# Kernel optimization log

Hardware: AMD Instinct MI355X
Metric: run time of the kernel (lower is better)

## Reference

```python
import jax, jax.numpy as jnp
import numpy as np

# Multi-level grid resolutions (module constants from init_kwargs)
RESO_3D = [16, 32, 64]
RESO_2D = [64, 128, 256]
EPS = 1e-9


def _corners(D):
    # binary corner offsets, shape (2**D, D)
    c = np.stack(np.meshgrid(*([np.arange(2)] * D), indexing='ij'), axis=-1).reshape(-1, D)
    return jnp.asarray(c, dtype=jnp.int32)


def _coords_weights(xyz, reso):
    # xyz in [0,1), shape (N, D). Returns flat voxel idx (N, 2**D) and trilinear weights (N, 2**D).
    D = xyz.shape[1]
    corners = _corners(D)                                   # (C, D)
    x = xyz * (reso - 1)
    x0 = jnp.floor(x)
    frac = x - x0                                           # (N, D)
    x0 = x0.astype(jnp.int32)
    cc = jnp.clip(x0[:, None, :] + corners[None], 0, reso - 1)   # (N, C, D)
    w = jnp.prod(jnp.where(corners[None] == 1, frac[:, None, :], 1.0 - frac[:, None, :]), axis=-1)  # (N, C)
    strides = (reso ** jnp.arange(D - 1, -1, -1)).astype(jnp.int32)  # row-major
    idx = jnp.sum(cc * strides, axis=-1)                    # (N, C)
    return idx, w


def _grid_create(xyz, feat, reso):
    # Scatter-splat: weighted-average point features into a dense level grid (reso**D, F).
    N, D = xyz.shape
    F = feat.shape[1]
    idx, w = _coords_weights(xyz, reso)                     # (N, C)
    flat_idx = idx.reshape(-1)
    wf = jnp.zeros((reso ** D, F), dtype=feat.dtype).at[flat_idx].add(
        (w[..., None] * feat[:, None, :]).reshape(-1, F))
    ws = jnp.zeros((reso ** D,), dtype=feat.dtype).at[flat_idx].add(w.reshape(-1))
    return wf / jnp.maximum(ws, EPS)[:, None]


def _grid_encode(xyz, grid, reso):
    # Gather + trilinear interpolation from a dense level grid. Returns (M, F).
    idx, w = _coords_weights(xyz, reso)                     # (M, C)
    vals = grid[idx]                                        # (M, C, F)
    return jnp.sum(w[..., None] * vals, axis=1)


def _spatial_ctx(xyz_c, xyz_i, feat):
    outs = []
    # 3D multi-level grid
    for R in RESO_3D:
        g = _grid_create(xyz_c, feat, R)
        outs.append(_grid_encode(xyz_i, g, R))
    # triplane 2D grids: xy, xz, yz
    for dims in ((0, 1), (0, 2), (1, 2)):
        xc = xyz_c[:, list(dims)]
        xi = xyz_i[:, list(dims)]
        for R in RESO_2D:
            g = _grid_create(xc, feat, R)
            outs.append(_grid_encode(xi, g, R))
    return jnp.concatenate(outs, axis=-1)  # (M, (L3 + 3*L2) * F)


def setup_inputs() -> dict:
    key = jax.random.key(0)
    k1, k2, k3 = jax.random.split(key, 3)
    N, M, F = 200000, 100000, 32
    xyz_for_creater = jax.random.uniform(k1, (N, 3), dtype=jnp.float32)
    xyz_for_interp = jax.random.uniform(k2, (M, 3), dtype=jnp.float32)
    feature = jax.random.normal(k3, (N, F), dtype=jnp.float32)
    return {"xyz_for_creater": xyz_for_creater,
            "xyz_for_interp": xyz_for_interp,
            "feature": feature}


def reference(xyz_for_creater, xyz_for_interp, feature):
    return _spatial_ctx(xyz_for_creater, xyz_for_interp, feature)
```

## Files before the change

kernel.cpp:

```cpp
#include <hip/hip_runtime.h>

#define NF 32
#define EPSF 1e-9f

#define KSORT 458752
#define VO16 0
#define VO32 4096
#define VO64Q 36864
#define VO128Q 49152
#define KVIS2 98304
#define KO16 0
#define KO32 4096
#define KO64 36864
#define KO64Q 299008
#define KO128Q 311296
#define KO256Q 360448
#define KVIS 557056

__device__ __forceinline__ int cell_coord(float xv, int R, float& fr) {
  float x = xv * (float)(R - 1);
  int i0 = (int)floorf(x);
  i0 = min(max(i0, 0), R - 2);
  fr = x - (float)i0;
  return i0;
}
__device__ __forceinline__ float bf2f(unsigned short u) {
  return __uint_as_float((unsigned)u << 16);
}
__device__ __forceinline__ unsigned short f2bf(float x) {
  unsigned b = __float_as_uint(x);
  return (unsigned short)((b + 0x7FFF + ((b >> 16) & 1)) >> 16);
}
__device__ __forceinline__ unsigned p1b2(unsigned x) {
  x &= 0x3FF;
  x = (x | (x << 16)) & 0x030000FF;
  x = (x | (x << 8)) & 0x0300F00F;
  x = (x | (x << 4)) & 0x030C30C3;
  x = (x | (x << 2)) & 0x09249249;
  return x;
}
__device__ __forceinline__ unsigned p1b1(unsigned x) {
  x &= 0xFFFF;
  x = (x | (x << 8)) & 0x00FF00FF;
  x = (x | (x << 4)) & 0x0F0F0F0F;
  x = (x | (x << 2)) & 0x33333333;
  x = (x | (x << 1)) & 0x55555555;
  return x;
}
__device__ __forceinline__ unsigned c1b2(unsigned x) {
  x &= 0x09249249u;
  x = (x | (x >> 2)) & 0x030C30C3u;
  x = (x | (x >> 4)) & 0x0300F00Fu;
  x = (x | (x >> 8)) & 0x030000FFu;
  x = (x | (x >> 16)) & 0x3FFu;
  return x;
}
__device__ __forceinline__ unsigned c1b1(unsigned x) {
  x &= 0x55555555u;
  x = (x | (x >> 1)) & 0x33333333u;
  x = (x | (x >> 2)) & 0x0F0F0F0Fu;
  x = (x | (x >> 4)) & 0x00FF00FFu;
  x = (x | (x >> 8)) & 0xFFFFu;
  return x;
}

__device__ __forceinline__ int xcd_swz(int bid, int n) {
  return (bid & 7) * (n >> 3) + (bid >> 3);
}

__device__ __forceinline__ void agg_hist(int key, int* cnt) {
  int lane = threadIdx.x & 63;
  unsigned long long amask = __ballot(1);
  int nact = __popcll(amask);
  int prev = __shfl_up(key, 1);
  bool leader = (lane == 0) || (prev != key);
  unsigned long long lmask = __ballot(leader);
  if (leader) {
    unsigned long long above = (lane < 63) ? (lmask >> (lane + 1)) : 0ULL;
    int next = above ? (lane + 1 + (__ffsll((unsigned long long)above) - 1)) : nact;
    atomicAdd(&cnt[key], next - lane);
  }
}
template <int NC>
__device__ __forceinline__ void agg_place_batch(const int (&key)[NC], int* cur,
                                                int (&pos)[NC]) {
  int lane = threadIdx.x & 63;
  unsigned long long amask = __ballot(1);
  int nact = __popcll(amask);
  int ret[NC];
  int lp[NC];
#pragma unroll
  for (int c = 0; c < NC; ++c) {
    int prev = __shfl_up(key[c], 1);
    bool leader = (lane == 0) || (prev != key[c]);
    unsigned long long lmask = __ballot(leader);
    unsigned long long below = lmask & ((2ULL << lane) - 1ULL);
    lp[c] = 63 - __clzll((long long)below);
    ret[c] = 0;
    if (leader) {
      unsigned long long above = (lane < 63) ? (lmask >> (lane + 1)) : 0ULL;
      int next = above ? (lane + 1 + (__ffsll((unsigned long long)above) - 1)) : nact;
      ret[c] = atomicAdd(&cur[key[c]], next - lane);
    }
  }
#pragma unroll
  for (int c = 0; c < NC; ++c) pos[c] = __shfl(ret[c], lp[c]) + (lane - lp[c]);
}

__global__ __launch_bounds__(256) void sort_hist_all(
    const float* __restrict__ xyz, int* __restrict__ cnt, int N) {
  int p = blockIdx.x * blockDim.x + threadIdx.x;
  if (p >= N) return;
  float fr;
  int c64[3], c256[3];
#pragma unroll
  for (int d = 0; d < 3; ++d) {
    c64[d] = cell_coord(xyz[p * 3 + d], 64, fr);
    c256[d] = cell_coord(xyz[p * 3 + d], 256, fr);
  }
  int k3 = (int)((p1b2((unsigned)c64[0]) << 2) | (p1b2((unsigned)c64[1]) << 1) |
                 p1b2((unsigned)c64[2]));
  atomicAdd(&cnt[k3], 1);
#pragma unroll
  for (int g = 0; g < 3; ++g) {
    int a = (g < 2) ? 0 : 1, b = (g == 0) ? 1 : 2;
    int key = 262144 + g * 65536 +
              (int)((p1b1((unsigned)c256[a]) << 1) | p1b1((unsigned)c256[b]));
    atomicAdd(&cnt[key], 1);
  }
}
__global__ __launch_bounds__(256) void sort_place_all(
    const float* __restrict__ xyz, int* __restrict__ cur, int* __restrict__ perm, int N) {
  int p = blockIdx.x * blockDim.x + threadIdx.x;
  if (p >= N) return;
  float fr;
  int c64[3], c256[3];
#pragma unroll
  for (int d = 0; d < 3; ++d) {
    c64[d] = cell_coord(xyz[p * 3 + d], 64, fr);
    c256[d] = cell_coord(xyz[p * 3 + d], 256, fr);
  }
  int k3 = (int)((p1b2((unsigned)c64[0]) << 2) | (p1b2((unsigned)c64[1]) << 1) |
                 p1b2((unsigned)c64[2]));
  perm[atomicAdd(&cur[k3], 1)] = p;
#pragma unroll
  for (int g = 0; g < 3; ++g) {
    int a = (g < 2) ? 0 : 1, b = (g == 0) ? 1 : 2;
    int key = 262144 + g * 65536 +
              (int)((p1b1((unsigned)c256[a]) << 1) | p1b1((unsigned)c256[b]));
    perm[atomicAdd(&cur[key], 1)] = p;
  }
}
__global__ __launch_bounds__(256) void permute_all(
    const float* __restrict__ xyz, const float* __restrict__ feat,
    const int* __restrict__ perm, float* __restrict__ xyz_s,
    unsigned short* __restrict__ feat_s, float* __restrict__ xy_g,
    unsigned short* __restrict__ feat_g, int N) {
  int t = blockIdx.x * blockDim.x + threadIdx.x;
  int s = t >> 5, f = t & 31;
  if (s >= 4 * N) return;
  int q = perm[s];
  float v = feat[(size_t)q * NF + f];
  if (s < N) {
    feat_s[(size_t)s * NF + f] = f2bf(v);
    if (f < 3) xyz_s[s * 3 + f] = xyz[q * 3 + f];
  } else {
    int sl = s - N;
    int g = sl / N;
    feat_g[(size_t)sl * NF + f] = f2bf(v);
    if (f < 2) {
      int a = (g < 2) ? 0 : 1, b = (g == 0) ? 1 : 2;
      xy_g[(size_t)sl * 2 + f] = xyz[q * 3 + (f == 0 ? a : b)];
    }
  }
}

__global__ __launch_bounds__(256) void scan_blocksum(
    const int* __restrict__ cnt, int* __restrict__ bsum, int K) {
  __shared__ int red[256];
  int base = blockIdx.x * 2048 + threadIdx.x * 8;
  int s = 0;
#pragma unroll
  for (int j = 0; j < 8; ++j) {
    int k = base + j;
    if (k < K) s += cnt[k];
  }
  red[threadIdx.x] = s;
  __syncthreads();
  for (int off = 128; off > 0; off >>= 1) {
    if (threadIdx.x < off) red[threadIdx.x] += red[threadIdx.x + off];
    __syncthreads();
  }
  if (threadIdx.x == 0) bsum[blockIdx.x] = red[0];
}
__global__ __launch_bounds__(256) void scan_write(
    const int* __restrict__ cnt, const int* __restrict__ bsum,
    int* __restrict__ cur, int K) {
  __shared__ int lds[256];
  __shared__ int boff;
  int b = blockIdx.x, t = threadIdx.x;
  if (t == 0) {
    int s = 0;
    for (int j = 0; j < b; ++j) s += bsum[j];
    boff = s;
  }
  int base = b * 2048 + t * 8;
  int v[8];
  int s = 0;
#pragma unroll
  for (int j = 0; j < 8; ++j) {
    int k = base + j;
    v[j] = (k < K) ? cnt[k] : 0;
    s += v[j];
  }
  lds[t] = s;
  __syncthreads();
  for (int off = 1; off < 256; off <<= 1) {
    int add = (t >= off) ? lds[t - off] : 0;
    __syncthreads();
    lds[t] += add;
    __syncthreads();
  }
  int run = boff + lds[t] - s;
#pragma unroll
  for (int j = 0; j < 8; ++j) {
    int k = base + j;
    if (k < K) {
      cur[k] = run;
      run += v[j];
    }
  }
}

__global__ __launch_bounds__(256) void hist_fused(
    const float* __restrict__ xyz_s, const float* __restrict__ xy_g,
    int* __restrict__ cnt, int N) {
  int y = blockIdx.y;
  int p = blockIdx.x * blockDim.x + threadIdx.x;
  if (p >= N) return;
  if (y < 2) {
    int R = 16 << y;
    int ko = (y == 0) ? VO16 : VO32;
    unsigned a0[3], a1[3];
    float fr[3];
#pragma unroll
    for (int d = 0; d < 3; ++d) {
      int i0 = cell_coord(xyz_s[p * 3 + d], R, fr[d]);
      a0[d] = p1b2((unsigned)i0);
      a1[d] = p1b2((unsigned)(i0 + 1));
    }
#pragma unroll
    for (int cb = 0; cb < 8; ++cb) {
      unsigned key = 0;
#pragma unroll
      for (int d = 0; d < 3; ++d) {
        int o = (cb >> d) & 1;
        key |= (o ? a1[d] : a0[d]) << (2 - d);
      }
      agg_hist(ko + (int)key, cnt);
    }
  } else {
    int idx = y - 2;
    int g = idx >> 1, r = idx & 1;
    int sl = g * N + p;
    int R = 64 << r;
    int kb = (r == 0) ? VO64Q : VO128Q;
    int base = kb + g * R * R;
    float frx, fry;
    int ix = cell_coord(xy_g[(size_t)sl * 2 + 0], R, frx);
    int iy = cell_coord(xy_g[(size_t)sl * 2 + 1], R, fry);
    unsigned ax0 = p1b1((unsigned)ix), ax1 = p1b1((unsigned)(ix + 1));
    unsigned ay0 = p1b1((unsigned)iy), ay1 = p1b1((unsigned)(iy + 1));
#pragma unroll
    for (int cb = 0; cb < 4; ++cb) {
      int o0 = (cb >> 1) & 1, o1 = cb & 1;
      agg_hist(base + (int)(((o0 ? ax1 : ax0) << 1) | (o1 ? ay1 : ay0)), cnt);
    }
  }
}

__global__ __launch_bounds__(256) void place_fused(
    const float* __restrict__ xyz_s, const float* __restrict__ xy_g,
    int* __restrict__ cur_v, int2* __restrict__ visits, int N) {
  int y = blockIdx.y;
  int p = blockIdx.x * blockDim.x + threadIdx.x;
  if (p >= N) return;
  if (y < 2) {
    int R = 16 << y;
    int ko = (y == 0) ? VO16 : VO32;
    unsigned a0[3], a1[3];
    float fr[3];
#pragma unroll
    for (int d = 0; d < 3; ++d) {
      int i0 = cell_coord(xyz_s[p * 3 + d], R, fr[d]);
      a0[d] = p1b2((unsigned)i0);
      a1[d] = p1b2((unsigned)(i0 + 1));
    }
    int keys[8];
    float ws[8];
#pragma unroll
    for (int cb = 0; cb < 8; ++cb) {
      float w = 1.f;
      unsigned key = 0;
#pragma unroll
      for (int d = 0; d < 3; ++d) {
        int o = (cb >> d) & 1;
        w *= o ? fr[d] : (1.f - fr[d]);
        key |= (o ? a1[d] : a0[d]) << (2 - d);
      }
      keys[cb] = ko + (int)key;
      ws[cb] = w;
    }
    int pos[8];
    agg_place_batch<8>(keys, cur_v, pos);
#pragma unroll
    for (int cb = 0; cb < 8; ++cb)
      visits[pos[cb]] = make_int2(p, __float_as_int(ws[cb]));
  } else {
    int idx = y - 2;
    int g = idx >> 1, r = idx & 1;
    int sl = g * N + p;
    int R = 64 << r;
    int kb = (r == 0) ? VO64Q : VO128Q;
    int base = kb + g * R * R;
    float frx, fry;
    int ix = cell_coord(xy_g[(size_t)sl * 2 + 0], R, frx);
    int iy = cell_coord(xy_g[(size_t)sl * 2 + 1], R, fry);
    unsigned ax0 = p1b1((unsigned)ix), ax1 = p1b1((unsigned)(ix + 1));
    unsigned ay0 = p1b1((unsigned)iy), ay1 = p1b1((unsigned)(iy + 1));
    int keys[4];
    float ws[4];
#pragma unroll
    for (int cb = 0; cb < 4; ++cb) {
      int o0 = (cb >> 1) & 1, o1 = cb & 1;
      ws[cb] = (o0 ? frx : 1.f - frx) * (o1 ? fry : 1.f - fry);
      keys[cb] = base + (int)(((o0 ? ax1 : ax0) << 1) | (o1 ? ay1 : ay0));
    }
    int pos[4];
    agg_place_batch<4>(keys, cur_v, pos);
#pragma unroll
    for (int cb = 0; cb < 4; ++cb)
      visits[pos[cb]] = make_int2(sl, __float_as_int(ws[cb]));
  }
}

__global__ __launch_bounds__(256) void stencil_coff(
    const int* __restrict__ cnt_all, const int* __restrict__ cur_all,
    int2* __restrict__ ccoff3, int2* __restrict__ ccoff2, int N) {
  int t = blockIdx.x * 256 + threadIdx.x;
  if (t < 262144) {
    int c = t;
    int cx = (int)c1b2((unsigned)c >> 2), cy = (int)c1b2((unsigned)c >> 1),
        cz = (int)c1b2((unsigned)c);
#pragma unroll
    for (int cb = 0; cb < 8; ++cb) {
      int hx = cx - (cb & 1), hy = cy - ((cb >> 1) & 1), hz = cz - ((cb >> 2) & 1);
      int n = 0, b = 0;
      if (hx >= 0 && hy >= 0 && hz >= 0) {
        int hk = (int)((p1b2((unsigned)hx) << 2) | (p1b2((unsigned)hy) << 1) |
                       p1b2((unsigned)hz));
        n = cnt_all[hk];
        b = cur_all[hk] - n;
      }
      ccoff3[(size_t)c * 8 + cb] = make_int2(b, n);
    }
  } else {
    int t2 = t - 262144;
    int g = t2 >> 16, m = t2 & 65535;
    int cx = (int)c1b1((unsigned)m >> 1), cy = (int)c1b1((unsigned)m);
    const int* cntg = cnt_all + 262144 + g * 65536;
    const int* curg = cur_all + 262144 + g * 65536;
#pragma unroll
    for (int cb = 0; cb < 4; ++cb) {
      int hx = cx - ((cb >> 1) & 1), hy = cy - (cb & 1);
      int n = 0, b = 0;
      if (hx >= 0 && hy >= 0) {
        int hk = (int)((p1b1((unsigned)hx) << 1) | p1b1((unsigned)hy));
        n = cntg[hk];
        b = curg[hk] - n - N;
      }
      ccoff2[(size_t)t2 * 4 + cb] = make_int2(b, n);
    }
  }
}

__global__ __launch_bounds__(256) void create_all_fused(
    const unsigned short* __restrict__ feat_s, const unsigned short* __restrict__ feat_g,
    const float* __restrict__ xyz_s, const float* __restrict__ xy_g,
    const int* __restrict__ cnt, const int* __restrict__ cur_end,
    const int2* __restrict__ visits, const int2* __restrict__ ccoff3,
    const int2* __restrict__ ccoff2, unsigned short* __restrict__ grid, int N) {
  __shared__ int2 vlds[1024];
  __shared__ float4 lacc4[256];
  __shared__ float lw[32];
  int bid = blockIdx.x;
  if (bid < 98304) {
    int vo, go, base, nseg;
    const unsigned short* feat;
    if (bid < 4096) {
      vo = VO16; go = KO16; base = 0; nseg = 4096; feat = feat_s;
    } else if (bid < 36864) {
      vo = VO32; go = KO32; base = 4096; nseg = 32768; feat = feat_s;
    } else if (bid < 49152) {
      vo = VO64Q; go = KO64Q; base = 36864; nseg = 12288; feat = feat_g;
    } else {
      vo = VO128Q; go = KO128Q; base = 49152; nseg = 49152; feat = feat_g;
    }
    int idx = xcd_swz(bid - base, nseg);
    int vcell = vo + idx;
    int e = cur_end[vcell];
    int n = cnt[vcell];
    int beg = e - n;
    for (int i = threadIdx.x; i < n && i < 1024; i += 256) vlds[i] = visits[beg + i];
    __syncthreads();
    bool inl = (n <= 1024);
    int slot = threadIdx.x >> 3;
    int fq = threadIdx.x & 7;
    float4 acc = {0.f, 0.f, 0.f, 0.f};
    float wsum = 0.f;
    int i = slot;
    for (; i + 32 < n; i += 64) {
      int2 v0 = inl ? vlds[i] : visits[beg + i];
      int2 v1 = inl ? vlds[i + 32] : visits[beg + i + 32];
      uint2 u0 = *(const uint2*)(feat + (size_t)v0.x * NF + 4 * fq);
      uint2 u1 = *(const uint2*)(feat + (size_t)v1.x * NF + 4 * fq);
      float w0 = __int_as_float(v0.y), w1 = __int_as_float(v1.y);
      acc.x = fmaf(w0, bf2f((unsigned short)u0.x), acc.x);
      acc.y = fmaf(w0, bf2f((unsigned short)(u0.x >> 16)), acc.y);
      acc.z = fmaf(w0, bf2f((unsigned short)u0.y), acc.z);
      acc.w = fmaf(w0, bf2f((unsigned short)(u0.y >> 16)), acc.w);
      acc.x = fmaf(w1, bf2f((unsigned short)u1.x), acc.x);
      acc.y = fmaf(w1, bf2f((unsigned short)(u1.x >> 16)), acc.y);
      acc.z = fmaf(w1, bf2f((unsigned short)u1.y), acc.z);
      acc.w = fmaf(w1, bf2f((unsigned short)(u1.y >> 16)), acc.w);
      wsum += w0 + w1;
    }
    if (i < n) {
      int2 v = inl ? vlds[i] : visits[beg + i];
      uint2 u = *(const uint2*)(feat + (size_t)v.x * NF + 4 * fq);
      float w = __int_as_float(v.y);
      acc.x = fmaf(w, bf2f((unsigned short)u.x), acc.x);
      acc.y = fmaf(w, bf2f((unsigned short)(u.x >> 16)), acc.y);
      acc.z = fmaf(w, bf2f((unsigned short)u.y), acc.z);
      acc.w = fmaf(w, bf2f((unsigned short)(u.y >> 16)), acc.w);
      wsum += w;
    }
    lacc4[threadIdx.x] = acc;
    if (fq == 0) lw[slot] = wsum;
    __syncthreads();
    if (threadIdx.x < 8) {
      float4 a = {0.f, 0.f, 0.f, 0.f};
      float w = 0.f;
#pragma unroll
      for (int s = 0; s < 32; ++s) {
        float4 t2 = lacc4[s * 8 + threadIdx.x];
        a.x += t2.x;
        a.y += t2.y;
        a.z += t2.z;
        a.w += t2.w;
        w += lw[s];
      }
      float inv = 1.f / fmaxf(w, EPSF);
      uint2 o;
      o.x = (unsigned)f2bf(a.x * inv) | ((unsigned)f2bf(a.y * inv) << 16);
      o.y = (unsigned)f2bf(a.z * inv) | ((unsigned)f2bf(a.w * inv) << 16);
      *(uint2*)(grid + (size_t)(go + idx) * NF + 4 * threadIdx.x) = o;
    }
    return;
  }
  int dbid = bid - 98304;
  int wave = threadIdx.x >> 6, lane = threadIdx.x & 63;
  int slot = lane >> 3;
  int fq = lane & 7;
  int2* wl = vlds + wave * 256;
  float4 acc = {0.f, 0.f, 0.f, 0.f};
  float wsum = 0.f;
  int gcell;
  const unsigned short* featp;
  if (dbid < 65536) {
    int cell = xcd_swz(dbid, 65536) * 4 + wave;
    gcell = KO64 + cell;
    featp = feat_s;
    int cx = (int)c1b2((unsigned)cell >> 2);
    int cy = (int)c1b2((unsigned)cell >> 1);
    int cz = (int)c1b2((unsigned)cell);
    int beg[8], pre[8];
    int tot = 0;
#pragma unroll
    for (int cb = 0; cb < 8; ++cb) {
      int2 co = ccoff3[(size_t)cell * 8 + cb];
      pre[cb] = tot;
      beg[cb] = co.x;
      tot += co.y;
    }
    for (int cbase = 0; cbase < tot; cbase += 256) {
      int chunk = min(tot - cbase, 256);
      for (int i = lane; i < chunk; i += 64) {
        int ii = cbase + i;
        int cls = 0, b = beg[0], p0 = pre[0];
#pragma unroll
        for (int c2 = 1; c2 < 8; ++c2)
          if (ii >= pre[c2]) { cls = c2; b = beg[c2]; p0 = pre[c2]; }
        int q = b + (ii - p0);
        int hx = cx - (cls & 1), hy = cy - ((cls >> 1) & 1), hz = cz - ((cls >> 2) & 1);
        float frx = xyz_s[q * 3 + 0] * 63.0f - (float)hx;
        float fry = xyz_s[q * 3 + 1] * 63.0f - (float)hy;
        float frz = xyz_s[q * 3 + 2] * 63.0f - (float)hz;
        float w = ((cls & 1) ? frx : 1.f - frx) *
                  (((cls >> 1) & 1) ? fry : 1.f - fry) *
                  (((cls >> 2) & 1) ? frz : 1.f - frz);
        wl[i] = make_int2(q, __float_as_int(w));
      }
      for (int i = slot; i < chunk; i += 8) {
        int2 v = wl[i];
        uint2 u = *(const uint2*)(featp + (size_t)v.x * NF + 4 * fq);
        float w = __int_as_float(v.y);
        acc.x = fmaf(w, bf2f((unsigned short)u.x), acc.x);
        acc.y = fmaf(w, bf2f((unsigned short)(u.x >> 16)), acc.y);
        acc.z = fmaf(w, bf2f((unsigned short)u.y), acc.z);
        acc.w = fmaf(w, bf2f((unsigned short)(u.y >> 16)), acc.w);
        wsum += w;
      }
    }
  } else {
    int cl = xcd_swz(dbid - 65536, 49152) * 4 + wave;
    gcell = KO256Q + cl;
    featp = feat_g;
    int g = cl >> 16, m = cl & 65535;
    int cx = (int)c1b1((unsigned)m >> 1);
    int cy = (int)c1b1((unsigned)m);
    int beg[4], pre[4];
    int tot = 0;
#pragma unroll
    for (int cb = 0; cb < 4; ++cb) {
      int2 co = ccoff2[(size_t)cl * 4 + cb];
      pre[cb] = tot;
      beg[cb] = co.x;
      tot += co.y;
    }
    for (int cbase = 0; cbase < tot; cbase += 256) {
      int chunk = min(tot - cbase, 256);
      for (int i = lane; i < chunk; i += 64) {
        int ii = cbase + i;
        int cls = 0, b = beg[0], p0 = pre[0];
#pragma unroll
        for (int c2 = 1; c2 < 4; ++c2)
          if (ii >= pre[c2]) { cls = c2; b = beg[c2]; p0 = pre[c2]; }
        int q = b + (ii - p0);
        int hx = cx - ((cls >> 1) & 1), hy = cy - (cls & 1);
        float frx = xy_g[(size_t)q * 2 + 0] * 255.0f - (float)hx;
        float fry = xy_g[(size_t)q * 2 + 1] * 255.0f - (float)hy;
        float w = (((cls >> 1) & 1) ? frx : 1.f - frx) * ((cls & 1) ? fry : 1.f - fry);
        wl[i] = make_int2(q, __float_as_int(w));
      }
      for (int i = slot; i < chunk; i += 8) {
        int2 v = wl[i];
        uint2 u = *(const uint2*)(featp + (size_t)v.x * NF + 4 * fq);
        float w = __int_as_float(v.y);
        acc.x = fmaf(w, bf2f((unsigned short)u.x), acc.x);
        acc.y = fmaf(w, bf2f((unsigned short)(u.x >> 16)), acc.y);
        acc.z = fmaf(w, bf2f((unsigned short)u.y), acc.z);
        acc.w = fmaf(w, bf2f((unsigned short)(u.y >> 16)), acc.w);
        wsum += w;
      }
    }
  }
#pragma unroll
  for (int d = 8; d < 64; d <<= 1) {
    acc.x += __shfl_xor(acc.x, d);
    acc.y += __shfl_xor(acc.y, d);
    acc.z += __shfl_xor(acc.z, d);
    acc.w += __shfl_xor(acc.w, d);
    wsum += __shfl_xor(wsum, d);
  }
  if (slot == 0) {
    float inv = 1.f / fmaxf(wsum, EPSF);
    uint2 o;
    o.x = (unsigned)f2bf(acc.x * inv) | ((unsigned)f2bf(acc.y * inv) << 16);
    o.y = (unsigned)f2bf(acc.z * inv) | ((unsigned)f2bf(acc.w * inv) << 16);
    *(uint2*)(grid + (size_t)gcell * NF + 4 * fq) = o;
  }
}

__global__ __launch_bounds__(256) void encode_all(
    const float* __restrict__ xyz, const unsigned short* __restrict__ grid,
    float* __restrict__ out, int M) {
  int t = blockIdx.x * blockDim.x + threadIdx.x;
  int m = t >> 5, f = t & 31;
  if (m >= M) return;
  float X[3];
#pragma unroll
  for (int d = 0; d < 3; ++d) X[d] = xyz[m * 3 + d];
  {
    const int RS[3] = {16, 32, 64};
    const int KO[3] = {KO16, KO32, KO64};
#pragma unroll
    for (int r = 0; r < 3; ++r) {
      unsigned a0[3], a1[3];
      float fr[3];
#pragma unroll
      for (int d = 0; d < 3; ++d) {
        int i0 = cell_coord(X[d], RS[r], fr[d]);
        a0[d] = p1b2((unsigned)i0);
        a1[d] = p1b2((unsigned)(i0 + 1));
      }
      float acc = 0.f;
#pragma unroll
      for (int cb = 0; cb < 8; ++cb) {
        float w = 1.f;
        unsigned key = 0;
#pragma unroll
        for (int d = 0; d < 3; ++d) {
          int o = (cb >> d) & 1;
          w *= o ? fr[d] : (1.f - fr[d]);
          key |= (o ? a1[d] : a0[d]) << (2 - d);
        }
        acc = fmaf(w, bf2f(grid[(size_t)(KO[r] + (int)key) * NF + f]), acc);
      }
      out[(size_t)m * 384 + r * 32 + f] = acc;
    }
  }
  {
    const int RS[3] = {64, 128, 256};
    const int KB[3] = {KO64Q, KO128Q, KO256Q};
    const int RSQ[3] = {4096, 16384, 65536};
#pragma unroll
    for (int r = 0; r < 3; ++r) {
      unsigned b0[3], b1[3];
      float fr[3];
#pragma unroll
      for (int d = 0; d < 3; ++d) {
        int i0 = cell_coord(X[d], RS[r], fr[d]);
        b0[d] = p1b1((unsigned)i0);
        b1[d] = p1b1((unsigned)(i0 + 1));
      }
#pragma unroll
      for (int g = 0; g < 3; ++g) {
        int a = (g < 2) ? 0 : 1, b = (g == 0) ? 1 : 2;
        int base = KB[r] + g * RSQ[r];
        float acc = 0.f;
#pragma unroll
        for (int cb = 0; cb < 4; ++cb) {
          int o0 = (cb >> 1) & 1, o1 = cb & 1;
          float w = (o0 ? fr[a] : 1.f - fr[a]) * (o1 ? fr[b] : 1.f - fr[b]);
          int k = base + (int)(((o0 ? b1[a] : b0[a]) << 1) | (o1 ? b1[b] : b0[b]));
          acc = fmaf(w, bf2f(grid[(size_t)k * NF + f]), acc);
        }
        out[(size_t)m * 384 + (3 + g * 3 + r) * 32 + f] = acc;
      }
    }
  }
}

extern "C" void kernel_launch(void* const* d_in, const int* in_sizes, int n_in,
                              void* d_out, int out_size, void* d_ws, size_t ws_size,
                              hipStream_t stream) {
  const float* xyz_c = (const float*)d_in[0];
  const float* xyz_i = (const float*)d_in[1];
  const float* feat = (const float*)d_in[2];
  float* out = (float*)d_out;
  int N = in_sizes[0] / 3;
  int M = in_sizes[1] / 3;

  char* wsb = (char*)d_ws;
  size_t off = 0;
  auto al = [&](size_t bytes) {
    size_t o = off;
    off = (off + bytes + 255) & ~(size_t)255;
    return wsb + o;
  };
  const int KALL = KSORT + KVIS2;
  int* cnt_all = (int*)al((size_t)KALL * 4);
  int* cur_all = (int*)al((size_t)KALL * 4);
  int* bsum = (int*)al(4096);
  int* perm = (int*)al((size_t)4 * N * 4);
  float* xyz_s = (float*)al((size_t)N * 3 * 4);
  unsigned short* feat_s = (unsigned short*)al((size_t)N * NF * 2);
  float* xy_g = (float*)al((size_t)3 * N * 2 * 4);
  unsigned short* feat_g = (unsigned short*)al((size_t)3 * N * NF * 2);
  int2* visits = (int2*)al((size_t)40 * N * 8);
  unsigned short* grid = (unsigned short*)al((size_t)KVIS * NF * 2);
  int2* ccoff3 = (int2*)al((size_t)262144 * 8 * 8);
  int2* ccoff2 = (int2*)al((size_t)196608 * 4 * 8);

  int* cnt_v = cnt_all + KSORT;
  int* cur_v = cur_all + KSORT;

  int pb = (N + 255) / 256;
  int nbs = (KSORT + 2047) / 2048;
  int nbv = (KVIS2 + 2047) / 2048;

  hipMemsetAsync(cnt_all, 0, (size_t)KALL * 4, stream);

  sort_hist_all<<<pb, 256, 0, stream>>>(xyz_c, cnt_all, N);
  scan_blocksum<<<nbs, 256, 0, stream>>>(cnt_all, bsum, KSORT);
  scan_write<<<nbs, 256, 0, stream>>>(cnt_all, bsum, cur_all, KSORT);
  sort_place_all<<<pb, 256, 0, stream>>>(xyz_c, cur_all, perm, N);
  permute_all<<<(4 * N * 32 + 255) / 256, 256, 0, stream>>>(xyz_c, feat, perm, xyz_s,
                                                            feat_s, xy_g, feat_g, N);

  stencil_coff<<<KSORT / 256, 256, 0, stream>>>(cnt_all, cur_all, ccoff3, ccoff2, N);

  hist_fused<<<dim3(pb, 8), 256, 0, stream>>>(xyz_s, xy_g, cnt_v, N);
  scan_blocksum<<<nbv, 256, 0, stream>>>(cnt_v, bsum, KVIS2);
  scan_write<<<nbv, 256, 0, stream>>>(cnt_v, bsum, cur_v, KVIS2);
  place_fused<<<dim3(pb, 8), 256, 0, stream>>>(xyz_s, xy_g, cur_v, visits, N);

  create_all_fused<<<98304 + 114688, 256, 0, stream>>>(
      feat_s, feat_g, xyz_s, xy_g, cnt_v, cur_v, visits, ccoff3, ccoff2, grid, N);

  encode_all<<<(M * 32 + 255) / 256, 256, 0, stream>>>(xyz_i, grid, out, M);
}
```

Measured before the change: 762.5 us.

## Map one 8-lane group per cell in dense-grid stencil gather

Reworks the stencil-based grid creation path for the 64^3 and 256^2 levels so each 8-thread group handles one cell serially, replacing the one-wave-per-cell scheme that staged weights in LDS and reduced with cross-lane shuffles. Each block now covers 32 cells instead of 4, and the grid launch shrinks to match. This removes the LDS staging, the shuffle reduction and the lanes left idle on sparsely populated cells (about 3 points per 64^3 cell on average). In exchange each group walks its cell's points sequentially, so load imbalance and per-point latency are exposed within the group.

```diff
diff --git a/kernel.cpp b/kernel.cpp
--- a/kernel.cpp
+++ b/kernel.cpp
@@ -469,18 +469,14 @@
     return;
   }
   int dbid = bid - 98304;
-  int wave = threadIdx.x >> 6, lane = threadIdx.x & 63;
-  int slot = lane >> 3;
-  int fq = lane & 7;
-  int2* wl = vlds + wave * 256;
+  int g8 = threadIdx.x >> 3;
+  int fq = threadIdx.x & 7;
   float4 acc = {0.f, 0.f, 0.f, 0.f};
   float wsum = 0.f;
   int gcell;
-  const unsigned short* featp;
-  if (dbid < 65536) {
-    int cell = xcd_swz(dbid, 65536) * 4 + wave;
+  if (dbid < 8192) {
+    int cell = xcd_swz(dbid, 8192) * 32 + g8;
     gcell = KO64 + cell;
-    featp = feat_s;
     int cx = (int)c1b2((unsigned)cell >> 2);
     int cy = (int)c1b2((unsigned)cell >> 1);
     int cz = (int)c1b2((unsigned)cell);
@@ -493,39 +489,29 @@
       beg[cb] = co.x;
       tot += co.y;
     }
-    for (int cbase = 0; cbase < tot; cbase += 256) {
-      int chunk = min(tot - cbase, 256);
-      for (int i = lane; i < chunk; i += 64) {
-        int ii = cbase + i;
-        int cls = 0, b = beg[0], p0 = pre[0];
-#pragma unroll
-        for (int c2 = 1; c2 < 8; ++c2)
-          if (ii >= pre[c2]) { cls = c2; b = beg[c2]; p0 = pre[c2]; }
-        int q = b + (ii - p0);
-        int hx = cx - (cls & 1), hy = cy - ((cls >> 1) & 1), hz = cz - ((cls >> 2) & 1);
-        float frx = xyz_s[q * 3 + 0] * 63.0f - (float)hx;
-        float fry = xyz_s[q * 3 + 1] * 63.0f - (float)hy;
-        float frz = xyz_s[q * 3 + 2] * 63.0f - (float)hz;
-        float w = ((cls & 1) ? frx : 1.f - frx) *
-                  (((cls >> 1) & 1) ? fry : 1.f - fry) *
-                  (((cls >> 2) & 1) ? frz : 1.f - frz);
-        wl[i] = make_int2(q, __float_as_int(w));
-      }
-      for (int i = slot; i < chunk; i += 8) {
-        int2 v = wl[i];
-        uint2 u = *(const uint2*)(featp + (size_t)v.x * NF + 4 * fq);
-        float w = __int_as_float(v.y);
-        acc.x = fmaf(w, bf2f((unsigned short)u.x), acc.x);
-        acc.y = fmaf(w, bf2f((unsigned short)(u.x >> 16)), acc.y);
-        acc.z = fmaf(w, bf2f((unsigned short)u.y), acc.z);
-        acc.w = fmaf(w, bf2f((unsigned short)(u.y >> 16)), acc.w);
-        wsum += w;
-      }
+    for (int i = 0; i < tot; ++i) {
+      int cls = 0, b = beg[0], p0 = pre[0];
+#pragma unroll
+      for (int c2 = 1; c2 < 8; ++c2)
+        if (i >= pre[c2]) { cls = c2; b = beg[c2]; p0 = pre[c2]; }
+      int q = b + (i - p0);
+      int hx = cx - (cls & 1), hy = cy - ((cls >> 1) & 1), hz = cz - ((cls >> 2) & 1);
+      float frx = xyz_s[q * 3 + 0] * 63.0f - (float)hx;
+      float fry = xyz_s[q * 3 + 1] * 63.0f - (float)hy;
+      float frz = xyz_s[q * 3 + 2] * 63.0f - (float)hz;
+      float w = ((cls & 1) ? frx : 1.f - frx) *
+                (((cls >> 1) & 1) ? fry : 1.f - fry) *
+                (((cls >> 2) & 1) ? frz : 1.f - frz);
+      uint2 u = *(const uint2*)(feat_s + (size_t)q * NF + 4 * fq);
+      acc.x = fmaf(w, bf2f((unsigned short)u.x), acc.x);
+      acc.y = fmaf(w, bf2f((unsigned short)(u.x >> 16)), acc.y);
+      acc.z = fmaf(w, bf2f((unsigned short)u.y), acc.z);
+      acc.w = fmaf(w, bf2f((unsigned short)(u.y >> 16)), acc.w);
+      wsum += w;
     }
   } else {
-    int cl = xcd_swz(dbid - 65536, 49152) * 4 + wave;
+    int cl = xcd_swz(dbid - 8192, 6144) * 32 + g8;
     gcell = KO256Q + cl;
-    featp = feat_g;
     int g = cl >> 16, m = cl & 65535;
     int cx = (int)c1b1((unsigned)m >> 1);
     int cy = (int)c1b1((unsigned)m);
@@ -538,48 +524,29 @@
       beg[cb] = co.x;
       tot += co.y;
     }
-    for (int cbase = 0; cbase < tot; cbase += 256) {
-      int chunk = min(tot - cbase, 256);
-      for (int i = lane; i < chunk; i += 64) {
-        int ii = cbase + i;
-        int cls = 0, b = beg[0], p0 = pre[0];
-#pragma unroll
-        for (int c2 = 1; c2 < 4; ++c2)
-          if (ii >= pre[c2]) { cls = c2; b = beg[c2]; p0 = pre[c2]; }
-        int q = b + (ii - p0);
-        int hx = cx - ((cls >> 1) & 1), hy = cy - (cls & 1);
-        float frx = xy_g[(size_t)q * 2 + 0] * 255.0f - (float)hx;
-        float fry = xy_g[(size_t)q * 2 + 1] * 255.0f - (float)hy;
-        float w = (((cls >> 1) & 1) ? frx : 1.f - frx) * ((cls & 1) ? fry : 1.f - fry);
-        wl[i] = make_int2(q, __float_as_int(w));
-      }
-      for (int i = slot; i < chunk; i += 8) {
-        int2 v = wl[i];
-        uint2 u = *(const uint2*)(featp + (size_t)v.x * NF + 4 * fq);
-        float w = __int_as_float(v.y);
-        acc.x = fmaf(w, bf2f((unsigned short)u.x), acc.x);
-        acc.y = fmaf(w, bf2f((unsigned short)(u.x >> 16)), acc.y);
-        acc.z = fmaf(w, bf2f((unsigned short)u.y), acc.z);
-        acc.w = fmaf(w, bf2f((unsigned short)(u.y >> 16)), acc.w);
-        wsum += w;
-      }
-    }
-  }
-#pragma unroll
-  for (int d = 8; d < 64; d <<= 1) {
-    acc.x += __shfl_xor(acc.x, d);
-    acc.y += __shfl_xor(acc.y, d);
-    acc.z += __shfl_xor(acc.z, d);
-    acc.w += __shfl_xor(acc.w, d);
-    wsum += __shfl_xor(wsum, d);
-  }
-  if (slot == 0) {
-    float inv = 1.f / fmaxf(wsum, EPSF);
-    uint2 o;
-    o.x = (unsigned)f2bf(acc.x * inv) | ((unsigned)f2bf(acc.y * inv) << 16);
-    o.y = (unsigned)f2bf(acc.z * inv) | ((unsigned)f2bf(acc.w * inv) << 16);
-    *(uint2*)(grid + (size_t)gcell * NF + 4 * fq) = o;
-  }
+    for (int i = 0; i < tot; ++i) {
+      int cls = 0, b = beg[0], p0 = pre[0];
+#pragma unroll
+      for (int c2 = 1; c2 < 4; ++c2)
+        if (i >= pre[c2]) { cls = c2; b = beg[c2]; p0 = pre[c2]; }
+      int q = b + (i - p0);
+      int hx = cx - ((cls >> 1) & 1), hy = cy - (cls & 1);
+      float frx = xy_g[(size_t)q * 2 + 0] * 255.0f - (float)hx;
+      float fry = xy_g[(size_t)q * 2 + 1] * 255.0f - (float)hy;
+      float w = (((cls >> 1) & 1) ? frx : 1.f - frx) * ((cls & 1) ? fry : 1.f - fry);
+      uint2 u = *(const uint2*)(feat_g + (size_t)q * NF + 4 * fq);
+      acc.x = fmaf(w, bf2f((unsigned short)u.x), acc.x);
+      acc.y = fmaf(w, bf2f((unsigned short)(u.x >> 16)), acc.y);
+      acc.z = fmaf(w, bf2f((unsigned short)u.y), acc.z);
+      acc.w = fmaf(w, bf2f((unsigned short)(u.y >> 16)), acc.w);
+      wsum += w;
+    }
+  }
+  float inv = 1.f / fmaxf(wsum, EPSF);
+  uint2 o;
+  o.x = (unsigned)f2bf(acc.x * inv) | ((unsigned)f2bf(acc.y * inv) << 16);
+  o.y = (unsigned)f2bf(acc.z * inv) | ((unsigned)f2bf(acc.w * inv) << 16);
+  *(uint2*)(grid + (size_t)gcell * NF + 4 * fq) = o;
 }
 
 __global__ __launch_bounds__(256) void encode_all(
@@ -706,7 +673,7 @@
   scan_write<<<nbv, 256, 0, stream>>>(cnt_v, bsum, cur_v, KVIS2);
   place_fused<<<dim3(pb, 8), 256, 0, stream>>>(xyz_s, xy_g, cur_v, visits, N);
 
-  create_all_fused<<<98304 + 114688, 256, 0, stream>>>(
+  create_all_fused<<<98304 + 14336, 256, 0, stream>>>(
       feat_s, feat_g, xyz_s, xy_g, cnt_v, cur_v, visits, ccoff3, ccoff2, grid, N);
 
   encode_all<<<(M * 32 + 255) / 256, 256, 0, stream>>>(xyz_i, grid, out, M);
```

Result: faster. 694.3 us (median of 2 runs) (-8.9%).
